# Performance work log

Hardware: AMD Instinct MI355X
Metric: run time of the kernel (lower is better)

Reference implementation:

```python
import jax, jax.numpy as jnp
import numpy as np

B, S, I, H, O = 128, 2048, 256, 512, 256

def _xavier(key, shape):
    fan_out, fan_in = shape
    limit = float(np.sqrt(6.0 / (fan_in + fan_out)))
    return jax.random.uniform(key, shape, jnp.float32, -limit, limit)

def setup_inputs() -> dict:
    key = jax.random.key(0)
    ks = jax.random.split(key, 10)
    inp = {"x": jax.random.normal(ks[0], (B, S, I), jnp.float32)}
    # input-to-hidden weights (no bias), shape [H, I] as in nn.Linear
    inp["W_ix"] = _xavier(ks[1], (H, I))
    inp["W_fx"] = _xavier(ks[2], (H, I))
    inp["W_ox"] = _xavier(ks[3], (H, I))
    inp["W_gx"] = _xavier(ks[4], (H, I))
    # hidden-to-hidden weights [H, H] with biases
    inp["W_ih"] = _xavier(ks[5], (H, H)); inp["b_ih"] = jnp.zeros((H,), jnp.float32)
    inp["W_fh"] = _xavier(ks[6], (H, H)); inp["b_fh"] = jnp.ones((H,), jnp.float32)  # forget bias = 1.0
    inp["W_oh"] = _xavier(ks[7], (H, H)); inp["b_oh"] = jnp.zeros((H,), jnp.float32)
    inp["W_gh"] = _xavier(ks[8], (H, H)); inp["b_gh"] = jnp.zeros((H,), jnp.float32)
    # output projection [O, H] with bias
    inp["W_ph"] = _xavier(ks[9], (O, H)); inp["b_ph"] = jnp.zeros((O,), jnp.float32)
    return inp

def _lstm_forward(x, W_ix, W_fx, W_ox, W_gx, W_ih, b_ih, W_fh, b_fh, W_oh, b_oh, W_gh, b_gh, W_ph, b_ph):
    Bc, Sc, _ = x.shape
    Hc = W_ih.shape[0]
    # Precompute all input-to-hidden projections in 4 big GEMMs: [B,S,H] each
    xi = jnp.einsum('bsi,hi->bsh', x, W_ix)
    xf = jnp.einsum('bsi,hi->bsh', x, W_fx)
    xo = jnp.einsum('bsi,hi->bsh', x, W_ox)
    xg = jnp.einsum('bsi,hi->bsh', x, W_gx)
    # scan over time; carry (h, c)
    def step(carry, xs):
        h, c = carry
        xi_t, xf_t, xo_t, xg_t = xs
        g = jnp.tanh(xg_t + h @ W_gh.T + b_gh)
        i = jax.nn.sigmoid(xi_t + h @ W_ih.T + b_ih)
        f = jax.nn.sigmoid(xf_t + h @ W_fh.T + b_fh)
        o = jax.nn.sigmoid(xo_t + h @ W_oh.T + b_oh)
        c = g * i + c * f
        h = jnp.tanh(c) * o
        return (h, c), None
    h0 = jnp.zeros((Bc, Hc), x.dtype)
    c0 = jnp.zeros((Bc, Hc), x.dtype)
    # time-major for scan: [S,B,H]
    xs = (xi.swapaxes(0, 1), xf.swapaxes(0, 1), xo.swapaxes(0, 1), xg.swapaxes(0, 1))
    (h_t, _), _ = jax.lax.scan(step, (h0, c0), xs)
    return h_t @ W_ph.T + b_ph

def reference(x, W_ix, W_fx, W_ox, W_gx, W_ih, b_ih, W_fh, b_fh, W_oh, b_oh, W_gh, b_gh, W_ph, b_ph):
    return _lstm_forward(x, W_ix, W_fx, W_ox, W_gx, W_ih, b_ih, W_fh, b_fh, W_oh, b_oh, W_gh, b_gh, W_ph, b_ph)
```

## Files before the change

### kernel.cpp

```cpp
#include <hip/hip_runtime.h>
#include <hip/hip_bf16.h>


#define BBATCH 128
#define SSEQ   2048
#define IIN    256
#define HHID   512
#define OOUT   256
#define NWG    256
#define NPROD  64
#define JPW    8
#define GBATCH 32
#define KP     776
#define PRESTR 36
#define FSTRIDE 16

typedef __attribute__((ext_vector_type(8))) short bfrag;
typedef __attribute__((ext_vector_type(4))) float f32x4;

typedef unsigned long long u64;
typedef unsigned short u16;
typedef unsigned int u32;

__device__ __forceinline__ float bf2f(u16 u) {
    union { u32 b; float f; } x; x.b = ((u32)u) << 16; return x.f;
}
__device__ __forceinline__ u16 f2bf(float f) {
    union { float f; u32 b; } x; x.f = f;
    u32 r = x.b + 0x7FFFu + ((x.b >> 16) & 1u);
    return (u16)(r >> 16);
}
__device__ __forceinline__ float frcp(float v) { return __builtin_amdgcn_rcpf(v); }
__device__ __forceinline__ float sigm(float v) { return frcp(1.0f + __expf(-v)); }
__device__ __forceinline__ float tanh_fast(float v) {
    float a = fminf(fmaxf(v, -9.0f), 9.0f);
    float e = __expf(2.0f * a);
    return (e - 1.0f) * frcp(e + 1.0f);
}

__device__ __forceinline__ bfrag pack8(const float* p) {
    float4 a = *(const float4*)p, b = *(const float4*)(p + 4);
    bfrag r;
    r[0] = (short)f2bf(a.x); r[1] = (short)f2bf(a.y);
    r[2] = (short)f2bf(a.z); r[3] = (short)f2bf(a.w);
    r[4] = (short)f2bf(b.x); r[5] = (short)f2bf(b.y);
    r[6] = (short)f2bf(b.z); r[7] = (short)f2bf(b.w);
    return r;
}
__device__ __forceinline__ u64 pack4(float4 v) {
    return (u64)f2bf(v.x) | ((u64)f2bf(v.y) << 16)
         | ((u64)f2bf(v.z) << 32) | ((u64)f2bf(v.w) << 48);
}

__global__ void __launch_bounds__(256)
xconv_kernel(const void* __restrict__ x, const void* __restrict__ bfh,
             u16* __restrict__ xbf) {
    const bool m32 = (*(const u32*)bfh) == 0x3F800000u;
    const size_t total = (size_t)SSEQ * BBATCH * (IIN / 4);
    for (size_t idx = (size_t)blockIdx.x * blockDim.x + threadIdx.x; idx < total;
         idx += (size_t)gridDim.x * blockDim.x) {
        size_t o4 = idx * 4;
        size_t s = o4 >> 15;
        size_t r = o4 & 32767;
        size_t b = r >> 8;
        size_t i = r & 255;
        size_t src = (b * SSEQ + s) * IIN + i;
        u64 v;
        if (m32) v = pack4(*(const float4*)((const float*)x + src));
        else     v = *(const u64*)((const u16*)x + src);
        *(u64*)(xbf + o4) = v;
    }
}

__global__ void __launch_bounds__(256, 1)
lstm_kernel(const void* __restrict__ x,
            const void* __restrict__ Wix, const void* __restrict__ Wfx,
            const void* __restrict__ Wox, const void* __restrict__ Wgx,
            const void* __restrict__ Wih, const void* __restrict__ bih,
            const void* __restrict__ Wfh, const void* __restrict__ bfh,
            const void* __restrict__ Woh, const void* __restrict__ boh,
            const void* __restrict__ Wgh, const void* __restrict__ bgh,
            const void* __restrict__ Wph, const void* __restrict__ bph,
            const u16* __restrict__ xbf, int use_xbf,
            u16* __restrict__ hbuf, u32* __restrict__ flags,
            void* __restrict__ out)
{
    __shared__ __align__(16) short Al[GBATCH * KP];
    __shared__ float pre[GBATCH * PRESTR];
    __shared__ float biasl[32];

    const bool m32 = (*(const u32*)bfh) == 0x3F800000u;

    const int wg  = blockIdx.x;
    const int tid = threadIdx.x;
    const int hs  = wg & 63;
    const int bq  = wg >> 6;
    const int j0  = hs * JPW;
    const int b0g = bq * GBATCH;

    const void* Whp[4] = { Wih, Wfh, Woh, Wgh };
    const void* Wxp[4] = { Wix, Wfx, Wox, Wgx };
    const void* bp[4]  = { bih, bfh, boh, bgh };

    if (tid < 32) {
        int gate = tid >> 3, jj = tid & 7;
        biasl[tid] = m32 ? ((const float*)bp[gate])[j0 + jj]
                         : bf2f(((const u16*)bp[gate])[j0 + jj]);
    }

    const int lane  = tid & 63;
    const int wv    = tid >> 6;
    const int ln    = lane & 15;
    const int qd    = lane >> 4;
    const int mtile = wv >> 1;
    const int ntile = wv & 1;

    bfrag breg[24];
    {
        int ng_  = ntile * 16 + ln;
        int gate = ng_ >> 3, jj = ng_ & 7;
        if (m32) {
            const float* wh = (const float*)Whp[gate] + (j0 + jj) * HHID;
            const float* wx = (const float*)Wxp[gate] + (j0 + jj) * IIN;
            #pragma unroll
            for (int kk = 0; kk < 16; ++kk) breg[kk] = pack8(wh + kk * 32 + qd * 8);
            #pragma unroll
            for (int kk = 0; kk < 8; ++kk)  breg[16 + kk] = pack8(wx + kk * 32 + qd * 8);
        } else {
            const u16* wh = (const u16*)Whp[gate] + (j0 + jj) * HHID;
            const u16* wx = (const u16*)Wxp[gate] + (j0 + jj) * IIN;
            #pragma unroll
            for (int kk = 0; kk < 16; ++kk) breg[kk] = *(const bfrag*)(wh + kk * 32 + qd * 8);
            #pragma unroll
            for (int kk = 0; kk < 8; ++kk)  breg[16 + kk] = *(const bfrag*)(wx + kk * 32 + qd * 8);
        }
    }

    float creg = 0.0f;
    const int gb  = tid >> 3;
    const int gjj = tid & 7;

    __syncthreads();

    for (int t = 0; t < SSEQ; ++t) {
        u16* hcur        = hbuf + (t & 1) * (BBATCH * HHID);
        const u16* hprev = hbuf + ((t & 1) ^ 1) * (BBATCH * HHID);

        if (use_xbf) {
            u64 xr[8];
            #pragma unroll
            for (int i2 = 0; i2 < 8; ++i2) {
                int v_ = tid + i2 * 256, b_ = v_ >> 6, kc = v_ & 63;
                xr[i2] = *(const u64*)(xbf +
                             ((size_t)t * BBATCH + b0g + b_) * IIN + kc * 4);
            }
            #pragma unroll
            for (int i2 = 0; i2 < 8; ++i2) {
                int v_ = tid + i2 * 256, b_ = v_ >> 6, kc = v_ & 63;
                *(u64*)(&Al[b_ * KP + HHID + kc * 4]) = xr[i2];
            }
        } else if (m32) {
            float4 xf[8];
            #pragma unroll
            for (int i2 = 0; i2 < 8; ++i2) {
                int v_ = tid + i2 * 256, b_ = v_ >> 6, kc = v_ & 63;
                xf[i2] = *(const float4*)((const float*)x +
                             ((size_t)(b0g + b_) * SSEQ + t) * IIN + kc * 4);
            }
            #pragma unroll
            for (int i2 = 0; i2 < 8; ++i2) {
                int v_ = tid + i2 * 256, b_ = v_ >> 6, kc = v_ & 63;
                *(u64*)(&Al[b_ * KP + HHID + kc * 4]) = pack4(xf[i2]);
            }
        } else {
            u64 xr[8];
            #pragma unroll
            for (int i2 = 0; i2 < 8; ++i2) {
                int v_ = tid + i2 * 256, b_ = v_ >> 6, kc = v_ & 63;
                xr[i2] = *(const u64*)((const u16*)x +
                             ((size_t)(b0g + b_) * SSEQ + t) * IIN + kc * 4);
            }
            #pragma unroll
            for (int i2 = 0; i2 < 8; ++i2) {
                int v_ = tid + i2 * 256, b_ = v_ >> 6, kc = v_ & 63;
                *(u64*)(&Al[b_ * KP + HHID + kc * 4]) = xr[i2];
            }
        }

        if (t > 0) {
            if (tid < NPROD) {
                while (__hip_atomic_load(&flags[(bq * NPROD + tid) * FSTRIDE],
                                         __ATOMIC_ACQUIRE,
                                         __HIP_MEMORY_SCOPE_AGENT) < (u32)t) { }
            }
        }
        __syncthreads();

        u64 hreg[16];
        if (t > 0) {
            #pragma unroll
            for (int i2 = 0; i2 < 16; ++i2) {
                int u_ = tid + i2 * 256, b_ = u_ >> 7, kq = u_ & 127;
                hreg[i2] = __hip_atomic_load(
                    (const u64*)(hprev + (size_t)(b0g + b_) * HHID + kq * 4),
                    __ATOMIC_RELAXED, __HIP_MEMORY_SCOPE_AGENT);
            }
        } else {
            #pragma unroll
            for (int i2 = 0; i2 < 16; ++i2) hreg[i2] = 0ull;
        }
        #pragma unroll
        for (int i2 = 0; i2 < 16; ++i2) {
            int u_ = tid + i2 * 256, b_ = u_ >> 7, kq = u_ & 127;
            *(u64*)(&Al[b_ * KP + kq * 4]) = hreg[i2];
        }
        __syncthreads();

        {
            const short* Ab = &Al[(mtile * 16 + ln) * KP + qd * 8];
            f32x4 a0 = {0.f,0.f,0.f,0.f}, a1 = {0.f,0.f,0.f,0.f};
            f32x4 a2 = {0.f,0.f,0.f,0.f}, a3 = {0.f,0.f,0.f,0.f};
            #pragma unroll
            for (int kk = 0; kk < 24; kk += 4) {
                a0 = __builtin_amdgcn_mfma_f32_16x16x32_bf16(
                    *(const bfrag*)(Ab + (kk + 0) * 32), breg[kk + 0], a0, 0, 0, 0);
                a1 = __builtin_amdgcn_mfma_f32_16x16x32_bf16(
                    *(const bfrag*)(Ab + (kk + 1) * 32), breg[kk + 1], a1, 0, 0, 0);
                a2 = __builtin_amdgcn_mfma_f32_16x16x32_bf16(
                    *(const bfrag*)(Ab + (kk + 2) * 32), breg[kk + 2], a2, 0, 0, 0);
                a3 = __builtin_amdgcn_mfma_f32_16x16x32_bf16(
                    *(const bfrag*)(Ab + (kk + 3) * 32), breg[kk + 3], a3, 0, 0, 0);
            }
            f32x4 acc = (a0 + a1) + (a2 + a3);
            #pragma unroll
            for (int r = 0; r < 4; ++r)
                pre[(mtile * 16 + qd * 4 + r) * PRESTR + ntile * 16 + ln] = acc[r];
        }
        __syncthreads();

        {
            float pi = pre[gb * PRESTR + gjj]      + biasl[gjj];
            float pf = pre[gb * PRESTR + 8 + gjj]  + biasl[8 + gjj];
            float po = pre[gb * PRESTR + 16 + gjj] + biasl[16 + gjj];
            float pg = pre[gb * PRESTR + 24 + gjj] + biasl[24 + gjj];
            float iv = sigm(pi), fv = sigm(pf), ov = sigm(po);
            float gv = tanh_fast(pg);
            creg = gv * iv + creg * fv;
            float h = tanh_fast(creg) * ov;
            u32 hb = (u32)f2bf(h);
            u32 v1 = (u32)__shfl_down((int)hb, 1);
            u32 lo = hb | (v1 << 16);
            u32 hi = (u32)__shfl_down((int)lo, 2);
            if ((tid & 3) == 0) {
                u64 val = (u64)lo | ((u64)hi << 32);
                __hip_atomic_store(
                    (u64*)(hcur + (size_t)(b0g + gb) * HHID + j0 + gjj),
                    val, __ATOMIC_RELAXED, __HIP_MEMORY_SCOPE_AGENT);
            }
        }

        __syncthreads();
        if (tid == 0)
            __hip_atomic_store(&flags[wg * FSTRIDE], (u32)(t + 1),
                               __ATOMIC_RELEASE, __HIP_MEMORY_SCOPE_AGENT);
    }

    {
        if (tid < NPROD) {
            while (__hip_atomic_load(&flags[(bq * NPROD + tid) * FSTRIDE],
                                     __ATOMIC_ACQUIRE,
                                     __HIP_MEMORY_SCOPE_AGENT) < (u32)SSEQ) { }
        }
        __syncthreads();
        const u16* hT = hbuf + ((SSEQ - 1) & 1) * (BBATCH * HHID);
        int b_ = b0g + (hs >> 1);
        int oh = (hs & 1) * 128;
        int oo = tid & 127;
        int kh = tid >> 7;
        float a = 0.f;
        for (int k = kh * 256; k < kh * 256 + 256; k += 4) {
            u64 hv = __hip_atomic_load((const u64*)(hT + (size_t)b_ * HHID + k),
                                       __ATOMIC_RELAXED, __HIP_MEMORY_SCOPE_AGENT);
            #pragma unroll
            for (int e = 0; e < 4; ++e) {
                float hf = bf2f((u16)(hv >> (16 * e)));
                float w0 = m32 ? ((const float*)Wph)[(oh + oo) * HHID + k + e]
                               : bf2f(((const u16*)Wph)[(oh + oo) * HHID + k + e]);
                a += hf * w0;
            }
        }
        pre[tid] = a;
        __syncthreads();
        if (kh == 0) {
            float bv = m32 ? ((const float*)bph)[oh + oo]
                           : bf2f(((const u16*)bph)[oh + oo]);
            float sum = pre[oo] + pre[128 + oo] + bv;
            if (m32) ((float*)out)[(size_t)b_ * OOUT + oh + oo] = sum;
            else     ((u16*)out)[(size_t)b_ * OOUT + oh + oo]  = f2bf(sum);
        }
    }
}

extern "C" void kernel_launch(void* const* d_in, const int* in_sizes, int n_in,
                              void* d_out, int out_size, void* d_ws, size_t ws_size,
                              hipStream_t stream) {
    const size_t xbf_bytes = (size_t)SSEQ * BBATCH * IIN * 2;
    const size_t hb_bytes  = (size_t)2 * BBATCH * HHID * 2;
    const size_t fl_bytes  = (size_t)NWG * FSTRIDE * sizeof(u32);

    int use_xbf = 0;
    u16* xbf = (u16*)d_ws;
    u16* hbuf;
    u32* flags;
    if (ws_size >= xbf_bytes + hb_bytes + fl_bytes) {
        use_xbf = 1;
        hbuf  = (u16*)((char*)d_ws + xbf_bytes);
        flags = (u32*)((char*)d_ws + xbf_bytes + hb_bytes);
    } else {
        hbuf  = (u16*)d_ws;
        flags = (u32*)((char*)d_ws + hb_bytes);
    }
    hipMemsetAsync(flags, 0, fl_bytes, stream);

    if (use_xbf) {
        hipLaunchKernelGGL(xconv_kernel, dim3(2048), dim3(256), 0, stream,
                           d_in[0], d_in[8], xbf);
    }

    hipLaunchKernelGGL(lstm_kernel, dim3(NWG), dim3(256), 0, stream,
                       d_in[0], d_in[1], d_in[2], d_in[3], d_in[4],
                       d_in[5], d_in[6], d_in[7], d_in[8], d_in[9],
                       d_in[10], d_in[11], d_in[12], d_in[13], d_in[14],
                       xbf, use_xbf, hbuf, flags, d_out);
}
```

Baseline: 17.80 ms.

## Repartition LSTM into 8 batch domains with per-producer flag polling and blocked h layout

Each group of workgroups now covers 16 batch rows and 16 hidden units per workgroup, so only 32 producers sync per batch domain instead of 64. A single wavefront polls the producer flags and copies each producer's h block into LDS as soon as that producer has finished, rather than waiting for all of them and then doing one bulk load. The hidden state is stored in a producer-blocked layout so that each producer's slice is contiguous. This cuts how many workgroups each step waits on and overlaps waiting with copying, at the cost of less MFMA work per wavefront (one 16-row tile) and a serialized copy done by a single wavefront.

```diff
diff --git a/kernel.cpp b/kernel.cpp
--- a/kernel.cpp
+++ b/kernel.cpp
@@ -8,11 +8,12 @@
 #define HHID   512
 #define OOUT   256
 #define NWG    256
-#define NPROD  64
-#define JPW    8
-#define GBATCH 32
+#define NDOM   8
+#define NPROD  32
+#define DB     16
+#define JPW    16
 #define KP     776
-#define PRESTR 36
+#define PRESTR 72
 #define FSTRIDE 16
 
 typedef __attribute__((ext_vector_type(8))) short bfrag;
@@ -85,50 +86,47 @@
             u16* __restrict__ hbuf, u32* __restrict__ flags,
             void* __restrict__ out)
 {
-    __shared__ __align__(16) short Al[GBATCH * KP];
-    __shared__ float pre[GBATCH * PRESTR];
-    __shared__ float biasl[32];
+    __shared__ __align__(16) short Al[DB * KP];
+    __shared__ float pre[DB * PRESTR];
+    __shared__ float biasl[64];
 
     const bool m32 = (*(const u32*)bfh) == 0x3F800000u;
 
-    const int wg  = blockIdx.x;
-    const int tid = threadIdx.x;
-    const int hs  = wg & 63;
-    const int bq  = wg >> 6;
-    const int j0  = hs * JPW;
-    const int b0g = bq * GBATCH;
+    const int wg    = blockIdx.x;
+    const int tid   = threadIdx.x;
+    const int slice = wg & (NPROD - 1);
+    const int dom   = wg >> 5;
+    const int j0    = slice * JPW;
+    const int b0g   = dom * DB;
 
     const void* Whp[4] = { Wih, Wfh, Woh, Wgh };
     const void* Wxp[4] = { Wix, Wfx, Wox, Wgx };
     const void* bp[4]  = { bih, bfh, boh, bgh };
 
-    if (tid < 32) {
-        int gate = tid >> 3, jj = tid & 7;
+    if (tid < 64) {
+        int gate = tid >> 4, jj = tid & 15;
         biasl[tid] = m32 ? ((const float*)bp[gate])[j0 + jj]
                          : bf2f(((const u16*)bp[gate])[j0 + jj]);
     }
 
-    const int lane  = tid & 63;
-    const int wv    = tid >> 6;
-    const int ln    = lane & 15;
-    const int qd    = lane >> 4;
-    const int mtile = wv >> 1;
-    const int ntile = wv & 1;
+    const int lane = tid & 63;
+    const int wv   = tid >> 6;
+    const int ln   = lane & 15;
+    const int qd   = lane >> 4;
 
     bfrag breg[24];
     {
-        int ng_  = ntile * 16 + ln;
-        int gate = ng_ >> 3, jj = ng_ & 7;
+        int row = j0 + ln;
         if (m32) {
-            const float* wh = (const float*)Whp[gate] + (j0 + jj) * HHID;
-            const float* wx = (const float*)Wxp[gate] + (j0 + jj) * IIN;
+            const float* wh = (const float*)Whp[wv] + (size_t)row * HHID;
+            const float* wx = (const float*)Wxp[wv] + (size_t)row * IIN;
             #pragma unroll
             for (int kk = 0; kk < 16; ++kk) breg[kk] = pack8(wh + kk * 32 + qd * 8);
             #pragma unroll
             for (int kk = 0; kk < 8; ++kk)  breg[16 + kk] = pack8(wx + kk * 32 + qd * 8);
         } else {
-            const u16* wh = (const u16*)Whp[gate] + (j0 + jj) * HHID;
-            const u16* wx = (const u16*)Wxp[gate] + (j0 + jj) * IIN;
+            const u16* wh = (const u16*)Whp[wv] + (size_t)row * HHID;
+            const u16* wx = (const u16*)Wxp[wv] + (size_t)row * IIN;
             #pragma unroll
             for (int kk = 0; kk < 16; ++kk) breg[kk] = *(const bfrag*)(wh + kk * 32 + qd * 8);
             #pragma unroll
@@ -137,8 +135,8 @@
     }
 
     float creg = 0.0f;
-    const int gb  = tid >> 3;
-    const int gjj = tid & 7;
+    const int gb  = tid >> 4;
+    const int gjj = tid & 15;
 
     __syncthreads();
 
@@ -147,77 +145,90 @@
         const u16* hprev = hbuf + ((t & 1) ^ 1) * (BBATCH * HHID);
 
         if (use_xbf) {
-            u64 xr[8];
-            #pragma unroll
-            for (int i2 = 0; i2 < 8; ++i2) {
-                int v_ = tid + i2 * 256, b_ = v_ >> 6, kc = v_ & 63;
+            u64 xr[4];
+            #pragma unroll
+            for (int i2 = 0; i2 < 4; ++i2) {
+                int m = tid + i2 * 256, b_ = m >> 6, kc = m & 63;
                 xr[i2] = *(const u64*)(xbf +
                              ((size_t)t * BBATCH + b0g + b_) * IIN + kc * 4);
             }
             #pragma unroll
-            for (int i2 = 0; i2 < 8; ++i2) {
-                int v_ = tid + i2 * 256, b_ = v_ >> 6, kc = v_ & 63;
+            for (int i2 = 0; i2 < 4; ++i2) {
+                int m = tid + i2 * 256, b_ = m >> 6, kc = m & 63;
                 *(u64*)(&Al[b_ * KP + HHID + kc * 4]) = xr[i2];
             }
         } else if (m32) {
-            float4 xf[8];
-            #pragma unroll
-            for (int i2 = 0; i2 < 8; ++i2) {
-                int v_ = tid + i2 * 256, b_ = v_ >> 6, kc = v_ & 63;
+            float4 xf[4];
+            #pragma unroll
+            for (int i2 = 0; i2 < 4; ++i2) {
+                int m = tid + i2 * 256, b_ = m >> 6, kc = m & 63;
                 xf[i2] = *(const float4*)((const float*)x +
                              ((size_t)(b0g + b_) * SSEQ + t) * IIN + kc * 4);
             }
             #pragma unroll
-            for (int i2 = 0; i2 < 8; ++i2) {
-                int v_ = tid + i2 * 256, b_ = v_ >> 6, kc = v_ & 63;
+            for (int i2 = 0; i2 < 4; ++i2) {
+                int m = tid + i2 * 256, b_ = m >> 6, kc = m & 63;
                 *(u64*)(&Al[b_ * KP + HHID + kc * 4]) = pack4(xf[i2]);
             }
         } else {
-            u64 xr[8];
-            #pragma unroll
-            for (int i2 = 0; i2 < 8; ++i2) {
-                int v_ = tid + i2 * 256, b_ = v_ >> 6, kc = v_ & 63;
+            u64 xr[4];
+            #pragma unroll
+            for (int i2 = 0; i2 < 4; ++i2) {
+                int m = tid + i2 * 256, b_ = m >> 6, kc = m & 63;
                 xr[i2] = *(const u64*)((const u16*)x +
                              ((size_t)(b0g + b_) * SSEQ + t) * IIN + kc * 4);
             }
             #pragma unroll
+            for (int i2 = 0; i2 < 4; ++i2) {
+                int m = tid + i2 * 256, b_ = m >> 6, kc = m & 63;
+                *(u64*)(&Al[b_ * KP + HHID + kc * 4]) = xr[i2];
+            }
+        }
+
+        if (t > 0) {
+            if (wv == 0) {
+                const int p  = lane >> 1;
+                const int hf = lane & 1;
+                const u32* fp = &flags[(dom * NPROD + p) * FSTRIDE];
+                const u16* src = hprev + ((size_t)(dom * NPROD + p)) * (DB * JPW)
+                               + hf * 8 * JPW;
+                short* dst = &Al[(hf * 8) * KP + p * JPW];
+                const u64 me = 1ull << lane;
+                u64 pend = ~0ull;
+                while (true) {
+                    u32 f = __hip_atomic_load(fp, __ATOMIC_ACQUIRE,
+                                              __HIP_MEMORY_SCOPE_AGENT);
+                    u64 arrived = __ballot(f >= (u32)t) & pend;
+                    if (arrived & me) {
+                        u64 d[8][4];
+                        #pragma unroll
+                        for (int r = 0; r < 8; ++r)
+                            #pragma unroll
+                            for (int e = 0; e < 4; ++e)
+                                d[r][e] = __hip_atomic_load(
+                                    (const u64*)(src + r * JPW + e * 4),
+                                    __ATOMIC_RELAXED, __HIP_MEMORY_SCOPE_AGENT);
+                        #pragma unroll
+                        for (int r = 0; r < 8; ++r)
+                            #pragma unroll
+                            for (int e = 0; e < 4; ++e)
+                                *(u64*)(dst + r * KP + e * 4) = d[r][e];
+                    }
+                    pend &= ~arrived;
+                    if (pend == 0) break;
+                }
+            }
+        } else {
+            #pragma unroll
             for (int i2 = 0; i2 < 8; ++i2) {
-                int v_ = tid + i2 * 256, b_ = v_ >> 6, kc = v_ & 63;
-                *(u64*)(&Al[b_ * KP + HHID + kc * 4]) = xr[i2];
-            }
-        }
-
-        if (t > 0) {
-            if (tid < NPROD) {
-                while (__hip_atomic_load(&flags[(bq * NPROD + tid) * FSTRIDE],
-                                         __ATOMIC_ACQUIRE,
-                                         __HIP_MEMORY_SCOPE_AGENT) < (u32)t) { }
-            }
-        }
-        __syncthreads();
-
-        u64 hreg[16];
-        if (t > 0) {
-            #pragma unroll
-            for (int i2 = 0; i2 < 16; ++i2) {
-                int u_ = tid + i2 * 256, b_ = u_ >> 7, kq = u_ & 127;
-                hreg[i2] = __hip_atomic_load(
-                    (const u64*)(hprev + (size_t)(b0g + b_) * HHID + kq * 4),
-                    __ATOMIC_RELAXED, __HIP_MEMORY_SCOPE_AGENT);
-            }
-        } else {
-            #pragma unroll
-            for (int i2 = 0; i2 < 16; ++i2) hreg[i2] = 0ull;
-        }
-        #pragma unroll
-        for (int i2 = 0; i2 < 16; ++i2) {
-            int u_ = tid + i2 * 256, b_ = u_ >> 7, kq = u_ & 127;
-            *(u64*)(&Al[b_ * KP + kq * 4]) = hreg[i2];
+                int m = tid + i2 * 256, b_ = m >> 7, kq = m & 127;
+                *(u64*)(&Al[b_ * KP + kq * 4]) = 0ull;
+            }
         }
         __syncthreads();
 
         {
-            const short* Ab = &Al[(mtile * 16 + ln) * KP + qd * 8];
+            const short* Ab = &Al[ln * KP + qd * 8];
             f32x4 a0 = {0.f,0.f,0.f,0.f}, a1 = {0.f,0.f,0.f,0.f};
             f32x4 a2 = {0.f,0.f,0.f,0.f}, a3 = {0.f,0.f,0.f,0.f};
             #pragma unroll
@@ -234,15 +245,15 @@
             f32x4 acc = (a0 + a1) + (a2 + a3);
             #pragma unroll
             for (int r = 0; r < 4; ++r)
-                pre[(mtile * 16 + qd * 4 + r) * PRESTR + ntile * 16 + ln] = acc[r];
+                pre[(qd * 4 + r) * PRESTR + wv * 16 + ln] = acc[r];
         }
         __syncthreads();
 
         {
             float pi = pre[gb * PRESTR + gjj]      + biasl[gjj];
-            float pf = pre[gb * PRESTR + 8 + gjj]  + biasl[8 + gjj];
-            float po = pre[gb * PRESTR + 16 + gjj] + biasl[16 + gjj];
-            float pg = pre[gb * PRESTR + 24 + gjj] + biasl[24 + gjj];
+            float pf = pre[gb * PRESTR + 16 + gjj] + biasl[16 + gjj];
+            float po = pre[gb * PRESTR + 32 + gjj] + biasl[32 + gjj];
+            float pg = pre[gb * PRESTR + 48 + gjj] + biasl[48 + gjj];
             float iv = sigm(pi), fv = sigm(pf), ov = sigm(po);
             float gv = tanh_fast(pg);
             creg = gv * iv + creg * fv;
@@ -254,7 +265,8 @@
             if ((tid & 3) == 0) {
                 u64 val = (u64)lo | ((u64)hi << 32);
                 __hip_atomic_store(
-                    (u64*)(hcur + (size_t)(b0g + gb) * HHID + j0 + gjj),
+                    (u64*)(hcur + (size_t)(dom * NPROD + slice) * (DB * JPW)
+                           + gb * JPW + gjj),
                     val, __ATOMIC_RELAXED, __HIP_MEMORY_SCOPE_AGENT);
             }
         }
@@ -267,25 +279,29 @@
 
     {
         if (tid < NPROD) {
-            while (__hip_atomic_load(&flags[(bq * NPROD + tid) * FSTRIDE],
+            while (__hip_atomic_load(&flags[(dom * NPROD + tid) * FSTRIDE],
                                      __ATOMIC_ACQUIRE,
                                      __HIP_MEMORY_SCOPE_AGENT) < (u32)SSEQ) { }
         }
         __syncthreads();
         const u16* hT = hbuf + ((SSEQ - 1) & 1) * (BBATCH * HHID);
-        int b_ = b0g + (hs >> 1);
-        int oh = (hs & 1) * 128;
+        int bl = slice >> 1;
+        int b_ = dom * DB + bl;
+        int oh = (slice & 1) * 128;
         int oo = tid & 127;
         int kh = tid >> 7;
         float a = 0.f;
         for (int k = kh * 256; k < kh * 256 + 256; k += 4) {
-            u64 hv = __hip_atomic_load((const u64*)(hT + (size_t)b_ * HHID + k),
-                                       __ATOMIC_RELAXED, __HIP_MEMORY_SCOPE_AGENT);
+            int p = k >> 4, jj = k & 15;
+            u64 hv = __hip_atomic_load(
+                (const u64*)(hT + ((size_t)(dom * NPROD + p)) * (DB * JPW)
+                             + bl * JPW + jj),
+                __ATOMIC_RELAXED, __HIP_MEMORY_SCOPE_AGENT);
             #pragma unroll
             for (int e = 0; e < 4; ++e) {
                 float hf = bf2f((u16)(hv >> (16 * e)));
-                float w0 = m32 ? ((const float*)Wph)[(oh + oo) * HHID + k + e]
-                               : bf2f(((const u16*)Wph)[(oh + oo) * HHID + k + e]);
+                float w0 = m32 ? ((const float*)Wph)[(size_t)(oh + oo) * HHID + k + e]
+                               : bf2f(((const u16*)Wph)[(size_t)(oh + oo) * HHID + k + e]);
                 a += hf * w0;
             }
         }
```

Measured after the change: 21.07 ms. 1.18x slower.

## Replace per-workgroup flag polling with per-step atomic arrival counters

Applied to the files above, without the earlier changes.

The inter-workgroup barrier used to have 64 threads each poll one producer flag. It now uses one counter per batch quarter and time step: each workgroup atomically increments it on release, and a single thread spins until it reaches 64, followed by an acquire fence. Hidden-state loads and stores also become plain memory accesses instead of relaxed agent-scope atomics, relying on the fence for ordering. The aim is to cut the polling traffic and latency of the per-timestep barrier. The trade-offs are contention on one shared atomic and a larger counter array that must be zeroed before each launch.

```diff
diff --git a/kernel.cpp b/kernel.cpp
--- a/kernel.cpp
+++ b/kernel.cpp
@@ -13,7 +13,7 @@
 #define GBATCH 32
 #define KP     776
 #define PRESTR 36
-#define FSTRIDE 16
+#define CSTRIDE 4
 
 typedef __attribute__((ext_vector_type(8))) short bfrag;
 typedef __attribute__((ext_vector_type(4))) float f32x4;
@@ -82,7 +82,7 @@
             const void* __restrict__ Wgh, const void* __restrict__ bgh,
             const void* __restrict__ Wph, const void* __restrict__ bph,
             const u16* __restrict__ xbf, int use_xbf,
-            u16* __restrict__ hbuf, u32* __restrict__ flags,
+            u16* __restrict__ hbuf, u32* __restrict__ ctr,
             void* __restrict__ out)
 {
     __shared__ __align__(16) short Al[GBATCH * KP];
@@ -188,11 +188,13 @@
         }
 
         if (t > 0) {
-            if (tid < NPROD) {
-                while (__hip_atomic_load(&flags[(bq * NPROD + tid) * FSTRIDE],
-                                         __ATOMIC_ACQUIRE,
-                                         __HIP_MEMORY_SCOPE_AGENT) < (u32)t) { }
-            }
+            if (tid == 0) {
+                u32* cp = &ctr[((size_t)bq * SSEQ + (t - 1)) * CSTRIDE];
+                while (__hip_atomic_fetch_add(cp, 0u, __ATOMIC_RELAXED,
+                                              __HIP_MEMORY_SCOPE_AGENT)
+                       < (u32)NPROD) { }
+            }
+            __builtin_amdgcn_fence(__ATOMIC_ACQUIRE, "agent");
         }
         __syncthreads();
 
@@ -201,9 +203,7 @@
             #pragma unroll
             for (int i2 = 0; i2 < 16; ++i2) {
                 int u_ = tid + i2 * 256, b_ = u_ >> 7, kq = u_ & 127;
-                hreg[i2] = __hip_atomic_load(
-                    (const u64*)(hprev + (size_t)(b0g + b_) * HHID + kq * 4),
-                    __ATOMIC_RELAXED, __HIP_MEMORY_SCOPE_AGENT);
+                hreg[i2] = *(const u64*)(hprev + (size_t)(b0g + b_) * HHID + kq * 4);
             }
         } else {
             #pragma unroll
@@ -253,24 +253,24 @@
             u32 hi = (u32)__shfl_down((int)lo, 2);
             if ((tid & 3) == 0) {
                 u64 val = (u64)lo | ((u64)hi << 32);
-                __hip_atomic_store(
-                    (u64*)(hcur + (size_t)(b0g + gb) * HHID + j0 + gjj),
-                    val, __ATOMIC_RELAXED, __HIP_MEMORY_SCOPE_AGENT);
+                *(u64*)(hcur + (size_t)(b0g + gb) * HHID + j0 + gjj) = val;
             }
         }
 
         __syncthreads();
         if (tid == 0)
-            __hip_atomic_store(&flags[wg * FSTRIDE], (u32)(t + 1),
-                               __ATOMIC_RELEASE, __HIP_MEMORY_SCOPE_AGENT);
+            __hip_atomic_fetch_add(&ctr[((size_t)bq * SSEQ + t) * CSTRIDE], 1u,
+                                   __ATOMIC_RELEASE, __HIP_MEMORY_SCOPE_AGENT);
     }
 
     {
-        if (tid < NPROD) {
-            while (__hip_atomic_load(&flags[(bq * NPROD + tid) * FSTRIDE],
-                                     __ATOMIC_ACQUIRE,
-                                     __HIP_MEMORY_SCOPE_AGENT) < (u32)SSEQ) { }
-        }
+        if (tid == 0) {
+            u32* cp = &ctr[((size_t)bq * SSEQ + (SSEQ - 1)) * CSTRIDE];
+            while (__hip_atomic_fetch_add(cp, 0u, __ATOMIC_RELAXED,
+                                          __HIP_MEMORY_SCOPE_AGENT)
+                   < (u32)NPROD) { }
+        }
+        __builtin_amdgcn_fence(__ATOMIC_ACQUIRE, "agent");
         __syncthreads();
         const u16* hT = hbuf + ((SSEQ - 1) & 1) * (BBATCH * HHID);
         int b_ = b0g + (hs >> 1);
@@ -279,8 +279,7 @@
         int kh = tid >> 7;
         float a = 0.f;
         for (int k = kh * 256; k < kh * 256 + 256; k += 4) {
-            u64 hv = __hip_atomic_load((const u64*)(hT + (size_t)b_ * HHID + k),
-                                       __ATOMIC_RELAXED, __HIP_MEMORY_SCOPE_AGENT);
+            u64 hv = *(const u64*)(hT + (size_t)b_ * HHID + k);
             #pragma unroll
             for (int e = 0; e < 4; ++e) {
                 float hf = bf2f((u16)(hv >> (16 * e)));
@@ -306,21 +305,21 @@
                               hipStream_t stream) {
     const size_t xbf_bytes = (size_t)SSEQ * BBATCH * IIN * 2;
     const size_t hb_bytes  = (size_t)2 * BBATCH * HHID * 2;
-    const size_t fl_bytes  = (size_t)NWG * FSTRIDE * sizeof(u32);
+    const size_t ct_bytes  = (size_t)4 * SSEQ * CSTRIDE * sizeof(u32);
 
     int use_xbf = 0;
     u16* xbf = (u16*)d_ws;
     u16* hbuf;
-    u32* flags;
-    if (ws_size >= xbf_bytes + hb_bytes + fl_bytes) {
+    u32* ctr;
+    if (ws_size >= xbf_bytes + hb_bytes + ct_bytes) {
         use_xbf = 1;
-        hbuf  = (u16*)((char*)d_ws + xbf_bytes);
-        flags = (u32*)((char*)d_ws + xbf_bytes + hb_bytes);
+        hbuf = (u16*)((char*)d_ws + xbf_bytes);
+        ctr  = (u32*)((char*)d_ws + xbf_bytes + hb_bytes);
     } else {
-        hbuf  = (u16*)d_ws;
-        flags = (u32*)((char*)d_ws + hb_bytes);
-    }
-    hipMemsetAsync(flags, 0, fl_bytes, stream);
+        hbuf = (u16*)d_ws;
+        ctr  = (u32*)((char*)d_ws + hb_bytes);
+    }
+    hipMemsetAsync(ctr, 0, ct_bytes, stream);
 
     if (use_xbf) {
         hipLaunchKernelGGL(xconv_kernel, dim3(2048), dim3(256), 0, stream,
@@ -331,5 +330,5 @@
                        d_in[0], d_in[1], d_in[2], d_in[3], d_in[4],
                        d_in[5], d_in[6], d_in[7], d_in[8], d_in[9],
                        d_in[10], d_in[11], d_in[12], d_in[13], d_in[14],
-                       xbf, use_xbf, hbuf, flags, d_out);
-}
+                       xbf, use_xbf, hbuf, ctr, d_out);
+}
```

After: 29.92 ms. 1.68x slower.
